# Performance work log

Measured on AMD Instinct MI355X. Metric: run time of the kernel, lower is better.

The kernel has to match this reference:

```python
import jax, jax.numpy as jnp
import numpy as np
import math

B, S, D = 4, 1024, 1024
H, DH = 16, 64
DFF = 4 * D
NEG = -1e9


def _layernorm(x, g, b, eps=1e-5):
    mu = jnp.mean(x, axis=-1, keepdims=True)
    var = jnp.var(x, axis=-1, keepdims=True)
    return (x - mu) * jax.lax.rsqrt(var + eps) * g + b


def setup_inputs() -> dict:
    key = jax.random.key(0)
    ks = jax.random.split(key, 12)
    inp = {
        "input": jax.random.normal(ks[0], (B, S, D), dtype=jnp.float32),
        # additive causal mask: 0 on/below diagonal, -1e9 above
        "causal_mask": jnp.where(
            jnp.tril(jnp.ones((S, S), dtype=bool)), 0.0, NEG
        ).astype(jnp.float32)[None, None],
        # additive padding mask: last 64 tokens of each sequence are padding
        "padding_mask": jnp.where(jnp.arange(S) < S - 64, 0.0, NEG)
        .astype(jnp.float32)[None, None, None, :]
        .repeat(B, axis=0),
        "ln1_g": jnp.ones((D,), jnp.float32), "ln1_b": jnp.zeros((D,), jnp.float32),
        "ln2_g": jnp.ones((D,), jnp.float32), "ln2_b": jnp.zeros((D,), jnp.float32),
        "ln3_g": jnp.ones((D,), jnp.float32), "ln3_b": jnp.zeros((D,), jnp.float32),
        "Wq": jax.random.normal(ks[1], (D, H * DH), jnp.float32) * 0.02,
        "bq": jnp.zeros((H * DH,), jnp.float32),
        "Wk": jax.random.normal(ks[2], (D, H * DH), jnp.float32) * 0.02,
        "bk": jnp.zeros((H * DH,), jnp.float32),
        "Wv": jax.random.normal(ks[3], (D, H * DH), jnp.float32) * 0.02,
        "bv": jnp.zeros((H * DH,), jnp.float32),
        "Wo": jax.random.normal(ks[4], (H * DH, D), jnp.float32) * 0.02,
        "bo": jnp.zeros((D,), jnp.float32),
        "W1": jax.random.normal(ks[5], (D, DFF), jnp.float32) * 0.02,
        "b1": jnp.zeros((DFF,), jnp.float32),
        "W2": jax.random.normal(ks[6], (DFF, D), jnp.float32) * 0.02,
        "b2": jnp.zeros((D,), jnp.float32),
    }
    return inp


def reference(input, causal_mask, padding_mask,
              ln1_g, ln1_b, ln2_g, ln2_b, ln3_g, ln3_b,
              Wq, bq, Wk, bk, Wv, bv, Wo, bo, W1, b1, W2, b2):
    x = _layernorm(input, ln1_g, ln1_b)
    b, s, _ = x.shape

    def heads(y):  # [b,s,H*DH] -> [b,H,s,DH]
        return y.reshape(b, s, H, DH).transpose(0, 2, 1, 3)

    q = heads(x @ Wq + bq)
    k = heads(x @ Wk + bk)
    v = heads(x @ Wv + bv)

    logits = jnp.einsum('bhqd,bhkd->bhqk', q, k) / math.sqrt(DH)
    logits = logits + causal_mask + padding_mask
    probs = jax.nn.softmax(logits, axis=-1)
    attn = jnp.einsum('bhqk,bhkd->bhqd', probs, v)
    attn = attn.transpose(0, 2, 1, 3).reshape(b, s, H * DH)  # b s (h d)
    attn_out = attn @ Wo + bo

    x = x + _layernorm(attn_out, ln2_g, ln2_b)
    h = _layernorm(x, ln3_g, ln3_b)
    x = x + (jax.nn.gelu(h @ W1 + b1, approximate=False) @ W2 + b2)
    return x
```

## Files before the change

### kernel.cpp

```cpp
#include <hip/hip_runtime.h>
#include <hip/hip_bf16.h>

typedef __hip_bfloat16 bf16;
typedef __bf16 bf16x8 __attribute__((ext_vector_type(8)));
typedef float f32x4 __attribute__((ext_vector_type(4)));

#define DEV __device__ __forceinline__

DEV int swz(int r, int k) { return r * 64 + (k ^ ((r & 7) << 3)); }

#define GLOAD_LDS16(gaddr, laddr)                                              \
  __builtin_amdgcn_global_load_lds(                                            \
      (const __attribute__((address_space(1))) void*)(gaddr),                  \
      (__attribute__((address_space(3))) void*)(laddr), 16, 0, 0)

__global__ void prep_kernel(
    const float* __restrict__ Wq, const float* __restrict__ Wk,
    const float* __restrict__ Wv, const float* __restrict__ Wo,
    const float* __restrict__ W1, const float* __restrict__ W2,
    const float* __restrict__ bq, const float* __restrict__ bk,
    const float* __restrict__ bv,
    bf16* __restrict__ WqkvT, bf16* __restrict__ WoT,
    bf16* __restrict__ W1T, bf16* __restrict__ W2T, float* __restrict__ bqkv) {
  int bid = blockIdx.x;
  if (bid >= 12288) {
    int i = (bid - 12288) * 256 + threadIdx.y * 32 + threadIdx.x;
    if (i < 3072)
      bqkv[i] = i < 1024 ? bq[i] : (i < 2048 ? bk[i - 1024] : bv[i - 2048]);
    return;
  }
  const float* src; bf16* dst; int K, N, tb;
  if (bid < 4096) {
    int wsel = bid >> 10;
    src = wsel == 0 ? Wq : wsel == 1 ? Wk : wsel == 2 ? Wv : Wo;
    dst = wsel < 3 ? WqkvT + (size_t)wsel * 1048576 : WoT;
    K = 1024; N = 1024; tb = bid & 1023;
  } else if (bid < 8192) {
    src = W1; dst = W1T; K = 1024; N = 4096; tb = bid - 4096;
  } else {
    src = W2; dst = W2T; K = 4096; N = 1024; tb = bid - 8192;
  }
  int ntx = N >> 5;
  int bx = (tb % ntx) * 32, by = (tb / ntx) * 32;
  __shared__ bf16 t[32][33];
  int tx = threadIdx.x, ty = threadIdx.y;
#pragma unroll
  for (int j = 0; j < 32; j += 8)
    t[ty + j][tx] = __float2bfloat16(src[(size_t)(by + ty + j) * N + bx + tx]);
  __syncthreads();
#pragma unroll
  for (int j = 0; j < 32; j += 8)
    dst[(size_t)(bx + ty + j) * K + by + tx] = t[tx][ty + j];
}

__global__ __launch_bounds__(256) void ln1_kernel(
    const float* __restrict__ in, const float* __restrict__ g, const float* __restrict__ b,
    float* __restrict__ xo, bf16* __restrict__ xb) {
  int row = blockIdx.x, tid = threadIdx.x;
  int lane = tid & 63, w = tid >> 6;
  float4 v = reinterpret_cast<const float4*>(in + (size_t)row * 1024)[tid];
  float s = v.x + v.y + v.z + v.w;
  float sq = v.x * v.x + v.y * v.y + v.z * v.z + v.w * v.w;
#pragma unroll
  for (int m = 32; m; m >>= 1) { s += __shfl_xor(s, m); sq += __shfl_xor(sq, m); }
  __shared__ float ss[4], qq[4];
  if (lane == 0) { ss[w] = s; qq[w] = sq; }
  __syncthreads();
  s = ss[0] + ss[1] + ss[2] + ss[3];
  sq = qq[0] + qq[1] + qq[2] + qq[3];
  float mu = s * (1.f / 1024.f);
  float rs = rsqrtf(sq * (1.f / 1024.f) - mu * mu + 1e-5f);
  float4 gg = reinterpret_cast<const float4*>(g)[tid];
  float4 bb = reinterpret_cast<const float4*>(b)[tid];
  float4 y;
  y.x = (v.x - mu) * rs * gg.x + bb.x;
  y.y = (v.y - mu) * rs * gg.y + bb.y;
  y.z = (v.z - mu) * rs * gg.z + bb.z;
  y.w = (v.w - mu) * rs * gg.w + bb.w;
  reinterpret_cast<float4*>(xo + (size_t)row * 1024)[tid] = y;
  union { bf16 h[4]; uint2 u; } pk;
  pk.h[0] = __float2bfloat16(y.x); pk.h[1] = __float2bfloat16(y.y);
  pk.h[2] = __float2bfloat16(y.z); pk.h[3] = __float2bfloat16(y.w);
  reinterpret_cast<uint2*>(xb + (size_t)row * 1024)[tid] = pk.u;
}

__global__ __launch_bounds__(256) void ln23_kernel(
    const float* __restrict__ x, const float* __restrict__ ao,
    const float* __restrict__ g2, const float* __restrict__ b2,
    const float* __restrict__ g3, const float* __restrict__ b3,
    float* __restrict__ x2o, bf16* __restrict__ hb) {
  int row = blockIdx.x, tid = threadIdx.x;
  int lane = tid & 63, w = tid >> 6;
  float4 a = reinterpret_cast<const float4*>(ao + (size_t)row * 1024)[tid];
  float s = a.x + a.y + a.z + a.w;
  float sq = a.x * a.x + a.y * a.y + a.z * a.z + a.w * a.w;
#pragma unroll
  for (int m = 32; m; m >>= 1) { s += __shfl_xor(s, m); sq += __shfl_xor(sq, m); }
  __shared__ float s1[4], q1[4], s2[4], q2[4];
  if (lane == 0) { s1[w] = s; q1[w] = sq; }
  __syncthreads();
  s = s1[0] + s1[1] + s1[2] + s1[3];
  sq = q1[0] + q1[1] + q1[2] + q1[3];
  float mu = s * (1.f / 1024.f);
  float rs = rsqrtf(sq * (1.f / 1024.f) - mu * mu + 1e-5f);
  float4 xr = reinterpret_cast<const float4*>(x + (size_t)row * 1024)[tid];
  float4 gg = reinterpret_cast<const float4*>(g2)[tid];
  float4 bb = reinterpret_cast<const float4*>(b2)[tid];
  float4 x2;
  x2.x = xr.x + (a.x - mu) * rs * gg.x + bb.x;
  x2.y = xr.y + (a.y - mu) * rs * gg.y + bb.y;
  x2.z = xr.z + (a.z - mu) * rs * gg.z + bb.z;
  x2.w = xr.w + (a.w - mu) * rs * gg.w + bb.w;
  reinterpret_cast<float4*>(x2o + (size_t)row * 1024)[tid] = x2;
  s = x2.x + x2.y + x2.z + x2.w;
  sq = x2.x * x2.x + x2.y * x2.y + x2.z * x2.z + x2.w * x2.w;
#pragma unroll
  for (int m = 32; m; m >>= 1) { s += __shfl_xor(s, m); sq += __shfl_xor(sq, m); }
  if (lane == 0) { s2[w] = s; q2[w] = sq; }
  __syncthreads();
  s = s2[0] + s2[1] + s2[2] + s2[3];
  sq = q2[0] + q2[1] + q2[2] + q2[3];
  mu = s * (1.f / 1024.f);
  rs = rsqrtf(sq * (1.f / 1024.f) - mu * mu + 1e-5f);
  gg = reinterpret_cast<const float4*>(g3)[tid];
  bb = reinterpret_cast<const float4*>(b3)[tid];
  union { bf16 h[4]; uint2 u; } pk;
  pk.h[0] = __float2bfloat16((x2.x - mu) * rs * gg.x + bb.x);
  pk.h[1] = __float2bfloat16((x2.y - mu) * rs * gg.y + bb.y);
  pk.h[2] = __float2bfloat16((x2.z - mu) * rs * gg.z + bb.z);
  pk.h[3] = __float2bfloat16((x2.w - mu) * rs * gg.w + bb.w);
  reinterpret_cast<uint2*>(hb + (size_t)row * 1024)[tid] = pk.u;
}

template <bool GELU, bool VSPLIT>
__global__ __launch_bounds__(512, 1) void gemm_8ph(
    const bf16* __restrict__ A, const bf16* __restrict__ BT,
    const float* __restrict__ bias, bf16* __restrict__ outb,
    bf16* __restrict__ kt, bf16* __restrict__ vt,
    int M, int N, int K) {
  __shared__ __align__(16) bf16 LDS[2][4][256 * 32];
  const int t = threadIdx.x, lane = t & 63, w = t >> 6;
  const int wr = w >> 2, wc = w & 3;
  const int l15 = lane & 15, l4 = lane >> 4;
  const int gx = gridDim.x, nwg = gx * gridDim.y;
  int bid = blockIdx.y * gx + blockIdx.x;
  int sbid = (bid & 7) * (nwg >> 3) + (bid >> 3);
  const int m0 = (sbid / gx) * 256, n0 = (sbid % gx) * 256;
  const int srow = lane >> 2;
  const int scol8 = (((lane & 3) ^ ((lane >> 3) & 3)) << 3);
  const int ldrd = l15 * 32 + ((l4 ^ ((l15 >> 1) & 3)) << 3);

  auto stage_half = [&](int buf, int tile, int h) {
    const bf16* P = (h & 1) ? BT : A;
    const int rb = (h & 1) ? n0 : m0;
    const int col = (tile << 6) + ((h >> 1) << 5) + scol8;
#pragma unroll
    for (int i = 0; i < 2; ++i) {
      int c = w * 2 + i;
      GLOAD_LDS16(P + (size_t)(rb + c * 16 + srow) * K + col, &LDS[buf][h][c * 512]);
    }
  };

  f32x4 acc[8][4] = {};
  bf16x8 bfr[4];

  auto mfma_phase = [&](int cb, int ks, int mh, bool loadB) {
    const bf16* Ah = &LDS[cb][ks * 2][0];
    if (loadB) {
      const bf16* Bh = &LDS[cb][ks * 2 + 1][0];
#pragma unroll
      for (int n = 0; n < 4; ++n)
        bfr[n] = *reinterpret_cast<const bf16x8*>(Bh + wc * 2048 + n * 512 + ldrd);
    }
    bf16x8 af[4];
#pragma unroll
    for (int m = 0; m < 4; ++m)
      af[m] = *reinterpret_cast<const bf16x8*>(Ah + wr * 4096 + mh * 2048 + m * 512 + ldrd);
    __builtin_amdgcn_s_setprio(1);
#pragma unroll
    for (int m = 0; m < 4; ++m)
#pragma unroll
      for (int n = 0; n < 4; ++n)
        acc[mh * 4 + m][n] =
            __builtin_amdgcn_mfma_f32_16x16x32_bf16(af[m], bfr[n], acc[mh * 4 + m][n], 0, 0, 0);
    __builtin_amdgcn_s_setprio(0);
  };

  const int nk = K >> 6;
#pragma unroll
  for (int h = 0; h < 4; ++h) stage_half(0, 0, h);

  for (int tt = 0; tt < nk - 1; ++tt) {
    const int cb = tt & 1;
    asm volatile("s_waitcnt vmcnt(4)" ::: "memory");
    asm volatile("s_barrier" ::: "memory");
    stage_half(cb ^ 1, tt + 1, 0);
    mfma_phase(cb, 0, 0, true);
    asm volatile("s_barrier" ::: "memory");
    stage_half(cb ^ 1, tt + 1, 1);
    mfma_phase(cb, 0, 1, false);
    asm volatile("s_waitcnt vmcnt(4)" ::: "memory");
    asm volatile("s_barrier" ::: "memory");
    stage_half(cb ^ 1, tt + 1, 2);
    mfma_phase(cb, 1, 0, true);
    asm volatile("s_barrier" ::: "memory");
    stage_half(cb ^ 1, tt + 1, 3);
    mfma_phase(cb, 1, 1, false);
  }
  {
    const int cb = (nk - 1) & 1;
    asm volatile("s_waitcnt vmcnt(4)" ::: "memory");
    asm volatile("s_barrier" ::: "memory");
    mfma_phase(cb, 0, 0, true);
    asm volatile("s_barrier" ::: "memory");
    mfma_phase(cb, 0, 1, false);
    asm volatile("s_waitcnt vmcnt(0)" ::: "memory");
    asm volatile("s_barrier" ::: "memory");
    mfma_phase(cb, 1, 0, true);
    asm volatile("s_barrier" ::: "memory");
    mfma_phase(cb, 1, 1, false);
  }

#pragma unroll
  for (int m = 0; m < 8; ++m) {
    int gr0 = m0 + wr * 128 + m * 16 + l4 * 4;
#pragma unroll
    for (int n = 0; n < 4; ++n) {
      int gc = n0 + wc * 64 + n * 16 + l15;
      float bv = bias[gc];
#pragma unroll
      for (int q = 0; q < 4; ++q) {
        int gr = gr0 + q;
        float v = acc[m][n][q] + bv;
        if constexpr (GELU) v = 0.5f * v * (1.f + erff(v * 0.70710678118654752f));
        if constexpr (VSPLIT) {
          int s = gr & 1023, bb = gr >> 10;
          if (gc < 1024) {
            outb[(size_t)gr * N + gc] = __float2bfloat16(v);
          } else if (gc < 2048) {
            int hd = gc - 1024, hh = hd >> 6, d = hd & 63;
            int ln = (s & 15) | (((d >> 3) & 3) << 4);
            kt[(((size_t)(bb * 16 + hh) * 64 + (s >> 4)) << 10) + (d >> 5) * 512 +
               ln * 8 + (d & 7)] = __float2bfloat16(v);
          } else {
            int hd = gc - 2048, hh = hd >> 6, d = hd & 63;
            int ln = (d & 15) | (((s >> 3) & 3) << 4);
            vt[(((size_t)(bb * 16 + hh) * 4 + (d >> 4)) << 14) + ((s >> 5) << 9) +
               ln * 8 + (s & 7)] = __float2bfloat16(v);
          }
        } else {
          outb[(size_t)gr * N + gc] = __float2bfloat16(v);
        }
      }
    }
  }
}

template <int BM, int BN, int WM, int WN, int MINW,
          bool GELU, bool RES, bool OUTBF>
__global__ __launch_bounds__(WM * WN * 64, MINW) void gemm_db(
    const bf16* __restrict__ A, const bf16* __restrict__ BT,
    const float* __restrict__ bias, const float* __restrict__ res,
    float* __restrict__ outf, bf16* __restrict__ outb,
    int M, int N, int K) {
  constexpr int NW = WM * WN;
  constexpr int MT = BM / WM / 16, NT = BN / WN / 16;
  constexpr int ACH = BM / 8, BCH = BN / 8;
  constexpr int PW = (ACH + BCH) / NW;
  __shared__ __align__(16) bf16 As[2][BM * 64];
  __shared__ __align__(16) bf16 Bs[2][BN * 64];
  const int t = threadIdx.x, lane = t & 63, w = t >> 6;
  const int wr = w / WN, wc = w % WN;
  const int l15 = lane & 15, l4 = lane >> 4;
  const int gx = gridDim.x, nwg = gx * gridDim.y;
  int bid = blockIdx.y * gx + blockIdx.x;
  int sbid = (bid & 7) * (nwg >> 3) + (bid >> 3);
  const int m0 = (sbid / gx) * BM, n0 = (sbid % gx) * BN;
  const int lr = lane >> 3;
  const int scol = ((lane & 7) * 8) ^ (lr * 8);

  auto stage = [&](int buf, int kt_) {
    const int k0 = kt_ << 6;
#pragma unroll
    for (int i = 0; i < PW; ++i) {
      int c = w * PW + i;
      if (c < ACH) {
        GLOAD_LDS16(A + (size_t)(m0 + c * 8 + lr) * K + k0 + scol, &As[buf][c * 512]);
      } else {
        int c2 = c - ACH;
        GLOAD_LDS16(BT + (size_t)(n0 + c2 * 8 + lr) * K + k0 + scol, &Bs[buf][c2 * 512]);
      }
    }
  };

  f32x4 acc[MT][NT] = {};
  const int nk = K >> 6;
  stage(0, 0);
  __syncthreads();
  int cur = 0;
  for (int kk = 0; kk < nk; ++kk) {
    if (kk + 1 < nk) stage(cur ^ 1, kk + 1);
#pragma unroll
    for (int ks = 0; ks < 2; ++ks) {
      bf16x8 af[MT], bfr[NT];
#pragma unroll
      for (int m = 0; m < MT; ++m)
        af[m] = *reinterpret_cast<const bf16x8*>(
            &As[cur][swz(wr * (BM / WM) + m * 16 + l15, ks * 32 + l4 * 8)]);
#pragma unroll
      for (int n = 0; n < NT; ++n)
        bfr[n] = *reinterpret_cast<const bf16x8*>(
            &Bs[cur][swz(wc * (BN / WN) + n * 16 + l15, ks * 32 + l4 * 8)]);
      __builtin_amdgcn_s_setprio(1);
#pragma unroll
      for (int m = 0; m < MT; ++m)
#pragma unroll
        for (int n = 0; n < NT; ++n)
          acc[m][n] = __builtin_amdgcn_mfma_f32_16x16x32_bf16(af[m], bfr[n], acc[m][n], 0, 0, 0);
      __builtin_amdgcn_s_setprio(0);
    }
    __syncthreads();
    cur ^= 1;
  }

#pragma unroll
  for (int m = 0; m < MT; ++m) {
    int gr0 = m0 + wr * (BM / WM) + m * 16 + l4 * 4;
#pragma unroll
    for (int n = 0; n < NT; ++n) {
      int gc = n0 + wc * (BN / WN) + n * 16 + l15;
      float bv = bias[gc];
#pragma unroll
      for (int q = 0; q < 4; ++q) {
        int gr = gr0 + q;
        float v = acc[m][n][q] + bv;
        if constexpr (GELU) v = 0.5f * v * (1.f + erff(v * 0.70710678118654752f));
        if constexpr (RES) v += res[(size_t)gr * N + gc];
        if constexpr (OUTBF) outb[(size_t)gr * N + gc] = __float2bfloat16(v);
        else                 outf[(size_t)gr * N + gc] = v;
      }
    }
  }
}

__global__ __launch_bounds__(256, 2) void attn_kernel(
    const bf16* __restrict__ qkv, const bf16* __restrict__ kt,
    const bf16* __restrict__ vt, bf16* __restrict__ o) {
  const int S = 1024, QS = 3072, HD = 1024;
  const bf16* qg = qkv;
  int bid = blockIdx.x;
  int xcd = bid & 7, j = bid >> 3;
  int grp = xcd * 8 + (j >> 3);
  int pr = j & 7;
  const int b = grp >> 4, h = grp & 15;
  const int t = threadIdx.x, lane = t & 63, w = t >> 6;
  const int l15 = lane & 15, l4 = lane >> 4;

  constexpr int PSTR = 72;
  __shared__ __align__(16) bf16 P[4][16 * PSTR];

  const int bh = b * 16 + h;
  const bf16* kbase = kt + ((size_t)bh << 16) + lane * 8;
  const bf16* vbase = vt + ((size_t)bh << 16) + lane * 8;

  bf16x8 kA[8], kB[8];
  auto loadK = [&](int kb, bf16x8* kf) {
#pragma unroll
    for (int cb = 0; cb < 4; ++cb)
#pragma unroll
      for (int ks = 0; ks < 2; ++ks)
        kf[cb * 2 + ks] = *reinterpret_cast<const bf16x8*>(
            kbase + (((kb >> 4) + cb) << 10) + (ks << 9));
  };

  auto run_strip = [&](int q0) {
    bf16x8 qf0, qf1;
    {
      const bf16* qp = qg + (size_t)(b * S + q0 + l15) * QS + h * 64 + l4 * 8;
      qf0 = *reinterpret_cast<const bf16x8*>(qp);
      qf1 = *reinterpret_cast<const bf16x8*>(qp + 32);
    }
    f32x4 acc[4] = {};
    float mrow = -1e30f, lrow = 0.f;
    const int kmaxa = q0 + 15, kmax = kmaxa < 959 ? kmaxa : 959;
    const int nt = (kmax >> 6) + 1;
    loadK(0, kA);

    for (int kt_ = 0; kt_ < nt; ++kt_) {
      const int kb = kt_ << 6;
      bf16x8* kf = (kt_ & 1) ? kB : kA;
      bf16x8* kn = (kt_ & 1) ? kA : kB;
      bf16x8 vf[8];
#pragma unroll
      for (int n = 0; n < 4; ++n)
#pragma unroll
        for (int ks = 0; ks < 2; ++ks)
          vf[n * 2 + ks] = *reinterpret_cast<const bf16x8*>(
              vbase + (n << 14) + (((kb >> 5) + ks) << 9));
      if (kt_ + 1 < nt) loadK(kb + 64, kn);

      f32x4 sc[4];
      __builtin_amdgcn_s_setprio(1);
#pragma unroll
      for (int cb = 0; cb < 4; ++cb) {
        f32x4 z = {};
        z = __builtin_amdgcn_mfma_f32_16x16x32_bf16(kf[cb * 2 + 0], qf0, z, 0, 0, 0);
        z = __builtin_amdgcn_mfma_f32_16x16x32_bf16(kf[cb * 2 + 1], qf1, z, 0, 0, 0);
        sc[cb] = z;
      }
      __builtin_amdgcn_s_setprio(0);

      const int q = q0 + l15;
      float p[16];
#pragma unroll
      for (int cb = 0; cb < 4; ++cb)
#pragma unroll
        for (int r = 0; r < 4; ++r) {
          int kgl = kb + cb * 16 + l4 * 4 + r;
          p[cb * 4 + r] = (kgl > q) ? -1e30f : sc[cb][r] * 0.125f;
        }
      float tm = p[0];
#pragma unroll
      for (int i = 1; i < 16; ++i) tm = fmaxf(tm, p[i]);
      tm = fmaxf(tm, __shfl_xor(tm, 16));
      tm = fmaxf(tm, __shfl_xor(tm, 32));
      bool defer = __all(tm <= mrow + 8.f);
      float mn = defer ? mrow : fmaxf(mrow, tm);
      float ps = 0.f;
#pragma unroll
      for (int i = 0; i < 16; ++i) { p[i] = __expf(p[i] - mn); ps += p[i]; }
      ps += __shfl_xor(ps, 16);
      ps += __shfl_xor(ps, 32);
      if (defer) {
        lrow += ps;
      } else {
        float al = __expf(mrow - mn);
        mrow = mn;
        lrow = lrow * al + ps;
#pragma unroll
        for (int n = 0; n < 4; ++n)
#pragma unroll
          for (int r = 0; r < 4; ++r) acc[n][r] *= al;
      }
#pragma unroll
      for (int cb = 0; cb < 4; ++cb) {
        union { bf16 h4[4]; uint2 u; } pk;
#pragma unroll
        for (int r = 0; r < 4; ++r) pk.h4[r] = __float2bfloat16(p[cb * 4 + r]);
        *reinterpret_cast<uint2*>(&P[w][l15 * PSTR + cb * 16 + l4 * 4]) = pk.u;
      }
      asm volatile("" ::: "memory");
      bf16x8 pb0 = *reinterpret_cast<const bf16x8*>(&P[w][l15 * PSTR + l4 * 8]);
      bf16x8 pb1 = *reinterpret_cast<const bf16x8*>(&P[w][l15 * PSTR + 32 + l4 * 8]);
      __builtin_amdgcn_s_setprio(1);
#pragma unroll
      for (int n = 0; n < 4; ++n) {
        acc[n] = __builtin_amdgcn_mfma_f32_16x16x32_bf16(vf[n * 2 + 0], pb0, acc[n], 0, 0, 0);
        acc[n] = __builtin_amdgcn_mfma_f32_16x16x32_bf16(vf[n * 2 + 1], pb1, acc[n], 0, 0, 0);
      }
      __builtin_amdgcn_s_setprio(0);
    }

    float inv = 1.f / lrow;
#pragma unroll
    for (int n = 0; n < 4; ++n) {
      union { bf16 h4[4]; uint2 u; } pk;
#pragma unroll
      for (int r = 0; r < 4; ++r) pk.h4[r] = __float2bfloat16(acc[n][r] * inv);
      *reinterpret_cast<uint2*>(&P[w][l15 * PSTR + n * 16 + l4 * 4]) = pk.u;
    }
    asm volatile("" ::: "memory");
    {
      int qq = lane >> 2, c = lane & 3;
#pragma unroll
      for (int i = 0; i < 2; ++i) {
        uint4 ov = *reinterpret_cast<const uint4*>(&P[w][qq * PSTR + c * 16 + i * 8]);
        *reinterpret_cast<uint4*>(
            o + (size_t)(b * S + q0 + qq) * HD + h * 64 + c * 16 + i * 8) = ov;
      }
    }
    asm volatile("" ::: "memory");
  };

  run_strip(pr * 64 + w * 16);
  run_strip((15 - pr) * 64 + w * 16);
}

extern "C" void kernel_launch(void* const* d_in, const int* in_sizes, int n_in,
                              void* d_out, int out_size, void* d_ws, size_t ws_size,
                              hipStream_t stream) {
  const float* input = (const float*)d_in[0];
  const float* ln1g = (const float*)d_in[3];
  const float* ln1b = (const float*)d_in[4];
  const float* ln2g = (const float*)d_in[5];
  const float* ln2b = (const float*)d_in[6];
  const float* ln3g = (const float*)d_in[7];
  const float* ln3b = (const float*)d_in[8];
  const float* Wq = (const float*)d_in[9];  const float* bq = (const float*)d_in[10];
  const float* Wk = (const float*)d_in[11]; const float* bk = (const float*)d_in[12];
  const float* Wv = (const float*)d_in[13]; const float* bv = (const float*)d_in[14];
  const float* Wo = (const float*)d_in[15]; const float* bo = (const float*)d_in[16];
  const float* W1 = (const float*)d_in[17]; const float* b1 = (const float*)d_in[18];
  const float* W2 = (const float*)d_in[19]; const float* b2 = (const float*)d_in[20];

  const int M = 4096, D = 1024, F = 4096;
  char* p = (char*)d_ws;
  size_t off = 0;
  auto nxt = [&](size_t n) { char* r = p + off; off += n; return r; };
  bf16* WqkvT = (bf16*)nxt((size_t)3 * D * D * 2);
  bf16* WoT = (bf16*)nxt((size_t)D * D * 2);
  bf16* W1T = (bf16*)nxt((size_t)F * D * 2);
  bf16* W2T = (bf16*)nxt((size_t)D * F * 2);
  float* bqkv = (float*)nxt(16384);
  float* xf  = (float*)nxt((size_t)M * D * 4);
  float* aof = (float*)nxt((size_t)M * D * 4);
  float* x2f = (float*)nxt((size_t)M * D * 4);
  bf16* xb = (bf16*)nxt((size_t)M * D * 2);
  bf16* qkv = (bf16*)nxt((size_t)M * 3 * D * 2);
  bf16* ktb = (bf16*)aof;
  bf16* vtb = (bf16*)((char*)aof + (size_t)8 * 1024 * 1024);
  bf16* gb = (bf16*)xf;
  bf16* ab = xb;
  bf16* hb = qkv;

  prep_kernel<<<12300, dim3(32, 8), 0, stream>>>(
      Wq, Wk, Wv, Wo, W1, W2, bq, bk, bv, WqkvT, WoT, W1T, W2T, bqkv);

  ln1_kernel<<<M, 256, 0, stream>>>(input, ln1g, ln1b, xf, xb);

  gemm_8ph<false, true><<<dim3(12, 16), 512, 0, stream>>>(
      xb, WqkvT, bqkv, qkv, ktb, vtb, M, 3 * D, D);

  attn_kernel<<<512, 256, 0, stream>>>(qkv, ktb, vtb, ab);

  gemm_db<128, 64, 2, 2, 4, false, false, false>
      <<<dim3(16, 32), 256, 0, stream>>>(
      ab, WoT, bo, nullptr, aof, nullptr, M, D, D);

  ln23_kernel<<<M, 256, 0, stream>>>(xf, aof, ln2g, ln2b, ln3g, ln3b, x2f, hb);

  gemm_8ph<true, false><<<dim3(16, 16), 512, 0, stream>>>(
      hb, W1T, b1, gb, nullptr, nullptr, M, F, D);
  gemm_db<128, 64, 2, 2, 4, false, true, false>
      <<<dim3(16, 32), 256, 0, stream>>>(
      gb, W2T, b2, x2f, (float*)d_out, nullptr, M, D, F);
}
```

Before: 222.8 us.

## Generalize 8-phase GEMM pipeline, reorder barriers, and use it for W2 projection

Templates the 8-phase GEMM on tile size and wave grid, and adds residual and fp32-output epilogues. Each phase now issues its LDS fragment reads before starting the next global-to-LDS stage, then runs a barrier and a scheduling fence before the MFMA block. The vmcnt waits and barriers move to the end of each phase, so loads and MFMAs overlap differently. The down-projection (W2) GEMM switches from the double-buffered 128x64 kernel to the 8-phase kernel with 128x128 tiles and 4 waves, which trades occupancy for more reuse per tile.

```diff
diff --git a/kernel.cpp b/kernel.cpp
--- a/kernel.cpp
+++ b/kernel.cpp
@@ -132,20 +132,25 @@
   reinterpret_cast<uint2*>(hb + (size_t)row * 1024)[tid] = pk.u;
 }
 
-template <bool GELU, bool VSPLIT>
-__global__ __launch_bounds__(512, 1) void gemm_8ph(
+template <int TS, int WM, int WN, bool GELU, bool RES, bool OUTBF, bool VSPLIT>
+__global__ __launch_bounds__(WM * WN * 64, 1) void gemm_8ph(
     const bf16* __restrict__ A, const bf16* __restrict__ BT,
-    const float* __restrict__ bias, bf16* __restrict__ outb,
+    const float* __restrict__ bias, const float* __restrict__ res,
+    float* __restrict__ outf, bf16* __restrict__ outb,
     bf16* __restrict__ kt, bf16* __restrict__ vt,
     int M, int N, int K) {
-  __shared__ __align__(16) bf16 LDS[2][4][256 * 32];
+  constexpr int NW = WM * WN;
+  constexpr int RH = TS / WM / 2;
+  constexpr int MT2 = RH / 16;
+  constexpr int NT = TS / WN / 16;
+  __shared__ __align__(16) bf16 LDS[2][4][TS * 32];
   const int t = threadIdx.x, lane = t & 63, w = t >> 6;
-  const int wr = w >> 2, wc = w & 3;
+  const int wr = w / WN, wc = w % WN;
   const int l15 = lane & 15, l4 = lane >> 4;
   const int gx = gridDim.x, nwg = gx * gridDim.y;
   int bid = blockIdx.y * gx + blockIdx.x;
   int sbid = (bid & 7) * (nwg >> 3) + (bid >> 3);
-  const int m0 = (sbid / gx) * 256, n0 = (sbid % gx) * 256;
+  const int m0 = (sbid / gx) * TS, n0 = (sbid % gx) * TS;
   const int srow = lane >> 2;
   const int scol8 = (((lane & 3) ^ ((lane >> 3) & 3)) << 3);
   const int ldrd = l15 * 32 + ((l4 ^ ((l15 >> 1) & 3)) << 3);
@@ -161,78 +166,72 @@
     }
   };
 
-  f32x4 acc[8][4] = {};
-  bf16x8 bfr[4];
-
-  auto mfma_phase = [&](int cb, int ks, int mh, bool loadB) {
+  f32x4 acc[2 * MT2][NT] = {};
+  bf16x8 bfr[NT];
+
+  auto phase = [&](int cb, int ks, int mh, int stg_tile, int stg_h, int vm) {
     const bf16* Ah = &LDS[cb][ks * 2][0];
-    if (loadB) {
+    if (mh == 0) {
       const bf16* Bh = &LDS[cb][ks * 2 + 1][0];
 #pragma unroll
-      for (int n = 0; n < 4; ++n)
-        bfr[n] = *reinterpret_cast<const bf16x8*>(Bh + wc * 2048 + n * 512 + ldrd);
-    }
-    bf16x8 af[4];
-#pragma unroll
-    for (int m = 0; m < 4; ++m)
-      af[m] = *reinterpret_cast<const bf16x8*>(Ah + wr * 4096 + mh * 2048 + m * 512 + ldrd);
+      for (int n = 0; n < NT; ++n)
+        bfr[n] = *reinterpret_cast<const bf16x8*>(Bh + (wc * (TS / WN) + n * 16) * 32 + ldrd);
+    }
+    bf16x8 af[MT2];
+#pragma unroll
+    for (int m = 0; m < MT2; ++m)
+      af[m] = *reinterpret_cast<const bf16x8*>(
+          Ah + (wr * (TS / WM) + mh * RH + m * 16) * 32 + ldrd);
+    if (stg_h >= 0) stage_half(cb ^ 1, stg_tile, stg_h);
+    asm volatile("s_barrier" ::: "memory");
+    __builtin_amdgcn_sched_barrier(0);
     __builtin_amdgcn_s_setprio(1);
 #pragma unroll
-    for (int m = 0; m < 4; ++m)
-#pragma unroll
-      for (int n = 0; n < 4; ++n)
-        acc[mh * 4 + m][n] =
-            __builtin_amdgcn_mfma_f32_16x16x32_bf16(af[m], bfr[n], acc[mh * 4 + m][n], 0, 0, 0);
+    for (int m = 0; m < MT2; ++m)
+#pragma unroll
+      for (int n = 0; n < NT; ++n)
+        acc[mh * MT2 + m][n] =
+            __builtin_amdgcn_mfma_f32_16x16x32_bf16(af[m], bfr[n], acc[mh * MT2 + m][n], 0, 0, 0);
     __builtin_amdgcn_s_setprio(0);
+    if (vm == 4) asm volatile("s_waitcnt vmcnt(4)" ::: "memory");
+    if (vm == 0) asm volatile("s_waitcnt vmcnt(0)" ::: "memory");
+    asm volatile("s_barrier" ::: "memory");
   };
 
   const int nk = K >> 6;
 #pragma unroll
   for (int h = 0; h < 4; ++h) stage_half(0, 0, h);
+  asm volatile("s_waitcnt vmcnt(4)" ::: "memory");
+  asm volatile("s_barrier" ::: "memory");
 
   for (int tt = 0; tt < nk - 1; ++tt) {
     const int cb = tt & 1;
-    asm volatile("s_waitcnt vmcnt(4)" ::: "memory");
-    asm volatile("s_barrier" ::: "memory");
-    stage_half(cb ^ 1, tt + 1, 0);
-    mfma_phase(cb, 0, 0, true);
-    asm volatile("s_barrier" ::: "memory");
-    stage_half(cb ^ 1, tt + 1, 1);
-    mfma_phase(cb, 0, 1, false);
-    asm volatile("s_waitcnt vmcnt(4)" ::: "memory");
-    asm volatile("s_barrier" ::: "memory");
-    stage_half(cb ^ 1, tt + 1, 2);
-    mfma_phase(cb, 1, 0, true);
-    asm volatile("s_barrier" ::: "memory");
-    stage_half(cb ^ 1, tt + 1, 3);
-    mfma_phase(cb, 1, 1, false);
+    phase(cb, 0, 0, tt + 1, 0, -1);
+    phase(cb, 0, 1, tt + 1, 1, 4);
+    phase(cb, 1, 0, tt + 1, 2, -1);
+    phase(cb, 1, 1, tt + 1, 3, 4);
   }
   {
     const int cb = (nk - 1) & 1;
-    asm volatile("s_waitcnt vmcnt(4)" ::: "memory");
-    asm volatile("s_barrier" ::: "memory");
-    mfma_phase(cb, 0, 0, true);
-    asm volatile("s_barrier" ::: "memory");
-    mfma_phase(cb, 0, 1, false);
-    asm volatile("s_waitcnt vmcnt(0)" ::: "memory");
-    asm volatile("s_barrier" ::: "memory");
-    mfma_phase(cb, 1, 0, true);
-    asm volatile("s_barrier" ::: "memory");
-    mfma_phase(cb, 1, 1, false);
-  }
-
-#pragma unroll
-  for (int m = 0; m < 8; ++m) {
-    int gr0 = m0 + wr * 128 + m * 16 + l4 * 4;
-#pragma unroll
-    for (int n = 0; n < 4; ++n) {
-      int gc = n0 + wc * 64 + n * 16 + l15;
+    phase(cb, 0, 0, 0, -1, -1);
+    phase(cb, 0, 1, 0, -1, 0);
+    phase(cb, 1, 0, 0, -1, -1);
+    phase(cb, 1, 1, 0, -1, -1);
+  }
+
+#pragma unroll
+  for (int mi = 0; mi < 2 * MT2; ++mi) {
+    int gr0 = m0 + wr * (TS / WM) + mi * 16 + l4 * 4;
+#pragma unroll
+    for (int n = 0; n < NT; ++n) {
+      int gc = n0 + wc * (TS / WN) + n * 16 + l15;
       float bv = bias[gc];
 #pragma unroll
       for (int q = 0; q < 4; ++q) {
         int gr = gr0 + q;
-        float v = acc[m][n][q] + bv;
+        float v = acc[mi][n][q] + bv;
         if constexpr (GELU) v = 0.5f * v * (1.f + erff(v * 0.70710678118654752f));
+        if constexpr (RES) v += res[(size_t)gr * N + gc];
         if constexpr (VSPLIT) {
           int s = gr & 1023, bb = gr >> 10;
           if (gc < 1024) {
@@ -248,8 +247,10 @@
             vt[(((size_t)(bb * 16 + hh) * 4 + (d >> 4)) << 14) + ((s >> 5) << 9) +
                ln * 8 + (s & 7)] = __float2bfloat16(v);
           }
+        } else if constexpr (OUTBF) {
+          outb[(size_t)gr * N + gc] = __float2bfloat16(v);
         } else {
-          outb[(size_t)gr * N + gc] = __float2bfloat16(v);
+          outf[(size_t)gr * N + gc] = v;
         }
       }
     }
@@ -528,8 +529,8 @@
 
   ln1_kernel<<<M, 256, 0, stream>>>(input, ln1g, ln1b, xf, xb);
 
-  gemm_8ph<false, true><<<dim3(12, 16), 512, 0, stream>>>(
-      xb, WqkvT, bqkv, qkv, ktb, vtb, M, 3 * D, D);
+  gemm_8ph<256, 2, 4, false, false, true, true><<<dim3(12, 16), 512, 0, stream>>>(
+      xb, WqkvT, bqkv, nullptr, nullptr, qkv, ktb, vtb, M, 3 * D, D);
 
   attn_kernel<<<512, 256, 0, stream>>>(qkv, ktb, vtb, ab);
 
@@ -539,9 +540,8 @@
 
   ln23_kernel<<<M, 256, 0, stream>>>(xf, aof, ln2g, ln2b, ln3g, ln3b, x2f, hb);
 
-  gemm_8ph<true, false><<<dim3(16, 16), 512, 0, stream>>>(
-      hb, W1T, b1, gb, nullptr, nullptr, M, F, D);
-  gemm_db<128, 64, 2, 2, 4, false, true, false>
-      <<<dim3(16, 32), 256, 0, stream>>>(
-      gb, W2T, b2, x2f, (float*)d_out, nullptr, M, D, F);
-}
+  gemm_8ph<256, 2, 4, true, false, true, false><<<dim3(16, 16), 512, 0, stream>>>(
+      hb, W1T, b1, nullptr, nullptr, gb, nullptr, nullptr, M, F, D);
+  gemm_8ph<128, 2, 2, false, true, false, false><<<dim3(8, 32), 256, 0, stream>>>(
+      gb, W2T, b2, x2f, (float*)d_out, nullptr, nullptr, nullptr, M, D, F);
+}
```

Measured after the change: 221.4 us. No clear change (-0.6%).
